# Kernel tuning notes

Measured on AMD Instinct MI355X. Metric: run time of the kernel, lower is better.

Reference implementation:

```python
import jax, jax.numpy as jnp
import numpy as np

DIM = 128
HEADS = 2
SR = 8
LN_EPS = 1e-5


def setup_inputs() -> dict:
    key = jax.random.key(0)
    ks = jax.random.split(key, 8)
    B, H, W, C = 8, 128, 128, DIM
    s = 0.02
    return {
        "x": jax.random.normal(ks[0], (B, H * W, C), jnp.float32),
        "h": H,
        "w": W,
        "Wq": jax.random.normal(ks[1], (C, C), jnp.float32) * s,
        "bq": jnp.zeros((C,), jnp.float32),
        "Wkv": jax.random.normal(ks[2], (2 * C, C), jnp.float32) * s,
        "bkv": jnp.zeros((2 * C,), jnp.float32),
        "Wp": jax.random.normal(ks[3], (C, C), jnp.float32) * s,
        "bp": jnp.zeros((C,), jnp.float32),
        "Wsr": jax.random.normal(ks[4], (C, C, SR, SR), jnp.float32) * s,  # OIHW
        "bsr": jnp.zeros((C,), jnp.float32),
        "gamma": jnp.ones((C,), jnp.float32),
        "beta": jnp.zeros((C,), jnp.float32),
    }


def reference(x, h, w, Wq, bq, Wkv, bkv, Wp, bp, Wsr, bsr, gamma, beta):
    b, n, c = x.shape
    hd = c // HEADS
    scale = hd ** -0.5
    # q: [b, heads, n, hd]
    q = (jnp.einsum('bnc,oc->bno', x, Wq) + bq).reshape(b, n, HEADS, hd).transpose(0, 2, 1, 3)
    # spatial reduction of k/v source: conv stride SR, then LayerNorm
    x_img = x.reshape(b, h, w, c).transpose(0, 3, 1, 2)  # NCHW
    xr = jax.lax.conv_general_dilated(
        x_img, Wsr, window_strides=(SR, SR), padding='VALID',
        dimension_numbers=('NCHW', 'OIHW', 'NCHW')) + bsr[None, :, None, None]
    xr = xr.reshape(b, c, -1).transpose(0, 2, 1)  # [b, m, c], m = (h/SR)*(w/SR)
    mu = jnp.mean(xr, axis=-1, keepdims=True)
    var = jnp.var(xr, axis=-1, keepdims=True)
    xr = (xr - mu) / jnp.sqrt(var + LN_EPS) * gamma + beta
    # k, v: [b, heads, m, hd]
    kv = jnp.einsum('bmc,oc->bmo', xr, Wkv) + bkv
    m = kv.shape[1]
    kv = kv.reshape(b, m, 2, HEADS, hd).transpose(2, 0, 3, 1, 4)
    k, v = kv[0], kv[1]
    attn = jax.nn.softmax(jnp.einsum('bhnd,bhmd->bhnm', q, k) * scale, axis=-1)
    out = jnp.einsum('bhnm,bhmd->bhnd', attn, v).transpose(0, 2, 1, 3).reshape(b, n, c)
    return jnp.einsum('bnc,oc->bno', out, Wp) + bp
```

## Files before the change

### kernel.cpp

```cpp
#include <hip/hip_runtime.h>
#include <stdint.h>

typedef __attribute__((ext_vector_type(8))) short bf16x8;
typedef __attribute__((ext_vector_type(4))) float f32x4;

#define MFMA16(A, B, C) __builtin_amdgcn_mfma_f32_16x16x32_bf16(A, B, C, 0, 0, 0)

static __device__ __forceinline__ unsigned short f2bf(float f) {
  uint32_t u = __float_as_uint(f);
  u = (u + 0x7fffu + ((u >> 16) & 1u)) >> 16;
  return (unsigned short)u;
}

static __device__ __forceinline__ bf16x8 pack8(float4 a, float4 b) {
  bf16x8 r;
  r[0] = (short)f2bf(a.x); r[1] = (short)f2bf(a.y);
  r[2] = (short)f2bf(a.z); r[3] = (short)f2bf(a.w);
  r[4] = (short)f2bf(b.x); r[5] = (short)f2bf(b.y);
  r[6] = (short)f2bf(b.z); r[7] = (short)f2bf(b.w);
  return r;
}

__global__ __launch_bounds__(256) void xcast_prep_kernel(
    const float* __restrict__ x, const float* __restrict__ Wq, const float* __restrict__ Wkv,
    const float* __restrict__ Wp, const float* __restrict__ Wsr,
    unsigned short* __restrict__ x2, unsigned short* __restrict__ x3,
    unsigned short* __restrict__ Wq2, unsigned short* __restrict__ Wkv2,
    unsigned short* __restrict__ Wp2, unsigned short* __restrict__ W2sr) {
  const int bid = blockIdx.x;
  const int tid = threadIdx.x;
  if (bid < 8192) {
    size_t t = (size_t)bid * 256 + tid;
    const float4* xp = (const float4*)(x + t * 8);
    bf16x8 v = pack8(xp[0], xp[1]);
    int n_all = (int)(t >> 4);
    int b = n_all >> 14, n = n_all & 16383;
    int c8 = (int)(t & 15);
    int c5 = c8 >> 2, c31 = (c8 & 3) * 8;
    size_t i2 = (size_t)b * 2097152 + ((size_t)((n >> 4) * 4 + c5)) * 512 + (n & 15) * 32 + c31;
    *(bf16x8*)(x2 + i2) = v;
    int y = n >> 7, xx = n & 127, jj = xx >> 3, kw = xx & 7;
    size_t i3 = (size_t)(b * 128 + y) * 16384 + ((size_t)(kw * 4 + c5)) * 512 + jj * 32 + c31;
    *(bf16x8*)(x3 + i3) = v;
    return;
  }
  if (bid < 8256) {
    int t = (bid - 8192) * 256 + tid;
    int o = t >> 7, c = t & 127;
    const float4* wp = (const float4*)(Wsr + (size_t)t * 64);
#pragma unroll
    for (int s4 = 0; s4 < 16; ++s4) {
      float4 v = wp[s4];
#pragma unroll
      for (int e = 0; e < 4; ++e) {
        int s = s4 * 4 + e;
        float f = (e == 0) ? v.x : (e == 1) ? v.y : (e == 2) ? v.z : v.w;
        W2sr[(size_t)((s * 4 + (c >> 5)) * 128 + o) * 32 + (c & 31)] = f2bf(f);
      }
    }
    return;
  }
  {
    int t = (bid - 8256) * 256 + tid;
    if (t < 16384) {
      int o = t >> 7, c = t & 127;
      Wq2[((c >> 5) * 128 + o) * 32 + (c & 31)] = f2bf(Wq[t]);
    } else if (t < 32768) {
      int u = t - 16384;
      int o = u >> 7, c = u & 127;
      Wp2[((c >> 5) * 128 + o) * 32 + (c & 31)] = f2bf(Wp[u]);
    } else {
      int u = t - 32768;
      int o = u >> 7, c = u & 127;
      Wkv2[((c >> 5) * 256 + o) * 32 + (c & 31)] = f2bf(Wkv[u]);
    }
  }
}

__global__ __launch_bounds__(256, 4) void conv_split_kernel(
    const unsigned short* __restrict__ x3, const unsigned short* __restrict__ W2sr,
    float* __restrict__ scratch) {
  const int tid = threadIdx.x;
  const int wave = tid >> 6, l = tid & 63, lg = l >> 4, lr = l & 15;
  const int pt = blockIdx.x;
  const int ks = blockIdx.y;

  __shared__ float red[4][16][128];

  const f32x4 zr = {0.f, 0.f, 0.f, 0.f};
  f32x4 acc[8];
#pragma unroll
  for (int ct = 0; ct < 8; ++ct) acc[ct] = zr;

  const int p = pt * 16;
  const int b = p >> 8, ii = (p >> 4) & 15;

  for (int kt = 0; kt < 16; ++kt) {
    const int k = ks * 2048 + wave * 512 + kt * 32;
    const int s = k >> 7, c0t = (k >> 5) & 3;
    const int kh = s >> 3, kw = s & 7, y = ii * 8 + kh;
    bf16x8 af = *(const bf16x8*)(x3 + (size_t)(b * 128 + y) * 16384 + (kw * 4 + c0t) * 512 + lr * 32 + lg * 8);
    const unsigned short* wb = W2sr + (size_t)(k >> 5) * 4096;
#pragma unroll
    for (int ct = 0; ct < 8; ++ct) {
      bf16x8 bfr = *(const bf16x8*)(wb + (ct * 16 + lr) * 32 + lg * 8);
      acc[ct] = MFMA16(af, bfr, acc[ct]);
    }
  }

#pragma unroll
  for (int ct = 0; ct < 8; ++ct)
#pragma unroll
    for (int r = 0; r < 4; ++r)
      red[wave][lg * 4 + r][ct * 16 + lr] = acc[ct][r];
  __syncthreads();

#pragma unroll
  for (int rr = 0; rr < 8; ++rr) {
    int idx = rr * 256 + tid;
    int row = idx >> 7, c = idx & 127;
    float v = red[0][row][c] + red[1][row][c] + red[2][row][c] + red[3][row][c];
    scratch[((size_t)(ks * 2048 + pt * 16 + row)) * 128 + c] = v;
  }
}

__global__ __launch_bounds__(256, 2) void ln_kv_kernel(
    const float* __restrict__ scratch, const float* __restrict__ bsr,
    const float* __restrict__ gamma, const float* __restrict__ beta,
    const unsigned short* __restrict__ Wkv2, const float* __restrict__ bkv,
    unsigned short* __restrict__ K2, unsigned short* __restrict__ V2) {
  const int tid = threadIdx.x;
  const int wave = tid >> 6, l = tid & 63, lg = l >> 4, lr = l & 15;
  const int blk = blockIdx.x;

  __shared__ unsigned short lns[16][136];

  {
    const int row = tid >> 4, c0 = (tid & 15) * 8;
    const int p = blk * 16 + row;
    float vals[8];
#pragma unroll
    for (int cc = 0; cc < 8; ++cc) vals[cc] = bsr[c0 + cc];
#pragma unroll
    for (int ksp = 0; ksp < 4; ++ksp) {
      const float4* sp = (const float4*)(scratch + ((size_t)(ksp * 2048 + p)) * 128 + c0);
      float4 a = sp[0], bb = sp[1];
      vals[0] += a.x; vals[1] += a.y; vals[2] += a.z; vals[3] += a.w;
      vals[4] += bb.x; vals[5] += bb.y; vals[6] += bb.z; vals[7] += bb.w;
    }
    float s1 = 0.f, s2 = 0.f;
#pragma unroll
    for (int cc = 0; cc < 8; ++cc) { s1 += vals[cc]; s2 += vals[cc] * vals[cc]; }
#pragma unroll
    for (int msk = 1; msk < 16; msk <<= 1) { s1 += __shfl_xor(s1, msk); s2 += __shfl_xor(s2, msk); }
    float mean = s1 * (1.f / 128.f);
    float var = s2 * (1.f / 128.f) - mean * mean;
    float rstd = rsqrtf(var + 1e-5f);
#pragma unroll
    for (int cc = 0; cc < 8; ++cc) {
      int c = c0 + cc;
      lns[row][c] = f2bf((vals[cc] - mean) * rstd * gamma[c] + beta[c]);
    }
  }
  __syncthreads();

  const f32x4 zr = {0.f, 0.f, 0.f, 0.f};
  f32x4 kv[4];
#pragma unroll
  for (int q = 0; q < 4; ++q) kv[q] = zr;
#pragma unroll
  for (int kt = 0; kt < 4; ++kt) {
    bf16x8 af = *(const bf16x8*)(&lns[lr][kt * 32 + lg * 8]);
#pragma unroll
    for (int q = 0; q < 4; ++q) {
      bf16x8 bfr = *(const bf16x8*)(Wkv2 + (kt * 256 + (wave * 4 + q) * 16 + lr) * 32 + lg * 8);
      kv[q] = MFMA16(af, bfr, kv[q]);
    }
  }
#pragma unroll
  for (int q = 0; q < 4; ++q)
#pragma unroll
    for (int r = 0; r < 4; ++r) {
      int o2 = (wave * 4 + q) * 16 + lr;
      int mrow = lg * 4 + r;
      int pp = blk * 16 + mrow;
      int bb = pp >> 8, mm = pp & 255;
      float val = kv[q][r] + bkv[o2];
      unsigned short hv = f2bf(val);
      if (o2 < 128) {
        int h = o2 >> 6, d = o2 & 63;
        K2[((size_t)((bb * 2 + h) * 2 + (d >> 5)) * 256 + mm) * 32 + (d & 31)] = hv;
      } else {
        int o3 = o2 - 128, h = o3 >> 6, d = o3 & 63;
        V2[((size_t)((bb * 2 + h) * 8 + (mm >> 5)) * 64 + d) * 32 + (mm & 31)] = hv;
      }
    }
}

__global__ __launch_bounds__(256, 3) void attn_kernel(
    const unsigned short* __restrict__ x2, const float* __restrict__ bq, const float* __restrict__ bp,
    const unsigned short* __restrict__ Wq2, const unsigned short* __restrict__ Wp2,
    const unsigned short* __restrict__ K2, const unsigned short* __restrict__ V2,
    float* __restrict__ out) {
  const int tid = threadIdx.x;
  const int wave = tid >> 6, l = tid & 63, lg = l >> 4, lr = l & 15;
  const int b = blockIdx.y;
  const int n0 = blockIdx.x * 64;

  __shared__ unsigned short Qs[64][136];
  __shared__ unsigned short Ps[4][16][272];

  const f32x4 zr = {0.f, 0.f, 0.f, 0.f};

  {
    const unsigned short* xbase = x2 + (size_t)b * 2097152 + (size_t)((n0 + wave * 16) >> 4) * 2048;
    bf16x8 af[4];
#pragma unroll
    for (int kt = 0; kt < 4; ++kt)
      af[kt] = *(const bf16x8*)(xbase + kt * 512 + lr * 32 + lg * 8);
    f32x4 qa[8];
#pragma unroll
    for (int ct = 0; ct < 8; ++ct) qa[ct] = zr;
#pragma unroll
    for (int kt = 0; kt < 4; ++kt) {
#pragma unroll
      for (int ct = 0; ct < 8; ++ct) {
        bf16x8 bfr = *(const bf16x8*)(Wq2 + (kt * 128 + ct * 16 + lr) * 32 + lg * 8);
        qa[ct] = MFMA16(af[kt], bfr, qa[ct]);
      }
    }
#pragma unroll
    for (int ct = 0; ct < 8; ++ct)
#pragma unroll
      for (int r = 0; r < 4; ++r) {
        int row = wave * 16 + lg * 4 + r;
        int col = ct * 16 + lr;
        Qs[row][col] = f2bf((qa[ct][r] + bq[col]) * 0.125f);
      }
  }
  __syncthreads();

  f32x4 oacc[2][4];
#pragma unroll
  for (int h2 = 0; h2 < 2; ++h2)
#pragma unroll
    for (int dt = 0; dt < 4; ++dt) oacc[h2][dt] = zr;

  for (int h = 0; h < 2; ++h) {
    f32x4 sacc[16];
#pragma unroll
    for (int mt = 0; mt < 16; ++mt) sacc[mt] = zr;
#pragma unroll
    for (int d0 = 0; d0 < 64; d0 += 32) {
      const unsigned short* kbase = K2 + (size_t)((b * 2 + h) * 2 + (d0 >> 5)) * 8192;
      bf16x8 qf = *(const bf16x8*)(&Qs[wave * 16 + lr][h * 64 + d0 + lg * 8]);
#pragma unroll
      for (int mt = 0; mt < 16; ++mt) {
        bf16x8 kf = *(const bf16x8*)(kbase + (mt * 16 + lr) * 32 + lg * 8);
        sacc[mt] = MFMA16(kf, qf, sacc[mt]);
      }
    }
    float mx = -1e30f;
#pragma unroll
    for (int mt = 0; mt < 16; ++mt)
#pragma unroll
      for (int r = 0; r < 4; ++r) mx = fmaxf(mx, sacc[mt][r]);
    mx = fmaxf(mx, __shfl_xor(mx, 16));
    mx = fmaxf(mx, __shfl_xor(mx, 32));
    float sum = 0.f;
#pragma unroll
    for (int mt = 0; mt < 16; ++mt)
#pragma unroll
      for (int r = 0; r < 4; ++r) {
        float pv = __expf(sacc[mt][r] - mx);
        sacc[mt][r] = pv; sum += pv;
      }
    sum += __shfl_xor(sum, 16);
    sum += __shfl_xor(sum, 32);
    float inv = 1.f / sum;
#pragma unroll
    for (int mt = 0; mt < 16; ++mt) {
      unsigned int w0 = (unsigned int)f2bf(sacc[mt][0] * inv) | ((unsigned int)f2bf(sacc[mt][1] * inv) << 16);
      unsigned int w1 = (unsigned int)f2bf(sacc[mt][2] * inv) | ((unsigned int)f2bf(sacc[mt][3] * inv) << 16);
      uint2 pw; pw.x = w0; pw.y = w1;
      *(uint2*)(&Ps[wave][lr][mt * 16 + lg * 4]) = pw;
    }

#pragma unroll
    for (int ki = 0; ki < 8; ++ki) {
      const unsigned short* vbase = V2 + (size_t)((b * 2 + h) * 8 + ki) * 2048;
      bf16x8 pf = *(const bf16x8*)(&Ps[wave][lr][ki * 32 + lg * 8]);
#pragma unroll
      for (int dt = 0; dt < 4; ++dt) {
        bf16x8 vf = *(const bf16x8*)(vbase + (dt * 16 + lr) * 32 + lg * 8);
        oacc[h][dt] = MFMA16(pf, vf, oacc[h][dt]);
      }
    }
  }

  __syncthreads();
  unsigned short* Op = &Ps[0][0][0];
#pragma unroll
  for (int h = 0; h < 2; ++h)
#pragma unroll
    for (int dt = 0; dt < 4; ++dt)
#pragma unroll
      for (int r = 0; r < 4; ++r) {
        int row = wave * 16 + lg * 4 + r;
        int col = h * 64 + dt * 16 + lr;
        Op[row * 136 + col] = f2bf(oacc[h][dt][r]);
      }

  f32x4 yacc[8];
#pragma unroll
  for (int ct = 0; ct < 8; ++ct) yacc[ct] = zr;
#pragma unroll
  for (int kt = 0; kt < 4; ++kt) {
    bf16x8 af = *(const bf16x8*)(&Op[(wave * 16 + lr) * 136 + kt * 32 + lg * 8]);
#pragma unroll
    for (int ct = 0; ct < 8; ++ct) {
      bf16x8 bfr = *(const bf16x8*)(Wp2 + (kt * 128 + ct * 16 + lr) * 32 + lg * 8);
      yacc[ct] = MFMA16(af, bfr, yacc[ct]);
    }
  }
#pragma unroll
  for (int ct = 0; ct < 8; ++ct)
#pragma unroll
    for (int r = 0; r < 4; ++r) {
      int n = n0 + wave * 16 + lg * 4 + r;
      int o = ct * 16 + lr;
      out[((size_t)(b * 16384 + n)) * 128 + o] = yacc[ct][r] + bp[o];
    }
}

extern "C" void kernel_launch(void* const* d_in, const int* in_sizes, int n_in,
                              void* d_out, int out_size, void* d_ws, size_t ws_size,
                              hipStream_t stream) {
  const float* x = (const float*)d_in[0];
  const float* Wq = (const float*)d_in[3];
  const float* bq = (const float*)d_in[4];
  const float* Wkv = (const float*)d_in[5];
  const float* bkv = (const float*)d_in[6];
  const float* Wp = (const float*)d_in[7];
  const float* bp = (const float*)d_in[8];
  const float* Wsr = (const float*)d_in[9];
  const float* bsr = (const float*)d_in[10];
  const float* gamma = (const float*)d_in[11];
  const float* beta = (const float*)d_in[12];
  float* out = (float*)d_out;

  unsigned short* ws = (unsigned short*)d_ws;
  unsigned short* Wq2 = ws;
  unsigned short* Wp2 = ws + 16384;
  unsigned short* Wkv2 = ws + 32768;
  unsigned short* W2sr = ws + 65536;
  unsigned short* K2 = ws + 1114112;
  unsigned short* V2 = ws + 1376256;
  unsigned short* x2 = ws + 1638400;
  unsigned short* x3 = ws + 18415616;
  float* scratch = (float*)(ws + 35192832);

  xcast_prep_kernel<<<8512, 256, 0, stream>>>(x, Wq, Wkv, Wp, Wsr, x2, x3, Wq2, Wkv2, Wp2, W2sr);
  conv_split_kernel<<<dim3(128, 4), 256, 0, stream>>>(x3, W2sr, scratch);
  ln_kv_kernel<<<128, 256, 0, stream>>>(scratch, bsr, gamma, beta, Wkv2, bkv, K2, V2);
  attn_kernel<<<dim3(256, 8), 256, 0, stream>>>(x2, bq, bp, Wq2, Wp2, K2, V2, out);
}
```

Measured before the change: 286.4 us.

## Drop bf16 x staging buffers; cast x in-kernel in conv and attention

Removes the prep pass that converted x into two bf16 layouts (x2, x3) in global memory. The conv and attention kernels now read fp32 x directly, convert it to bf16 in shared memory (with an XOR swizzle in conv), and the conv writes per-wave partial sums that ln_kv reduces over 16 splits. The attention kernel switches to per-wave shared buffers with lgkmcnt waits instead of block barriers, and stages the output through LDS for coalesced float4 stores. This saves about 64MB of intermediate writes and reads, at the cost of more scratch traffic and more LDS per conv block.

```diff
diff --git a/kernel.cpp b/kernel.cpp
--- a/kernel.cpp
+++ b/kernel.cpp
@@ -5,6 +5,9 @@
 typedef __attribute__((ext_vector_type(4))) float f32x4;
 
 #define MFMA16(A, B, C) __builtin_amdgcn_mfma_f32_16x16x32_bf16(A, B, C, 0, 0, 0)
+
+#define LGKM_GUARD() do { asm volatile("s_waitcnt lgkmcnt(0)" ::: "memory"); \
+                          __builtin_amdgcn_sched_barrier(0); } while (0)
 
 static __device__ __forceinline__ unsigned short f2bf(float f) {
   uint32_t u = __float_as_uint(f);
@@ -21,31 +24,15 @@
   return r;
 }
 
-__global__ __launch_bounds__(256) void xcast_prep_kernel(
-    const float* __restrict__ x, const float* __restrict__ Wq, const float* __restrict__ Wkv,
+__global__ __launch_bounds__(256) void prep_kernel(
+    const float* __restrict__ Wq, const float* __restrict__ Wkv,
     const float* __restrict__ Wp, const float* __restrict__ Wsr,
-    unsigned short* __restrict__ x2, unsigned short* __restrict__ x3,
     unsigned short* __restrict__ Wq2, unsigned short* __restrict__ Wkv2,
     unsigned short* __restrict__ Wp2, unsigned short* __restrict__ W2sr) {
   const int bid = blockIdx.x;
   const int tid = threadIdx.x;
-  if (bid < 8192) {
-    size_t t = (size_t)bid * 256 + tid;
-    const float4* xp = (const float4*)(x + t * 8);
-    bf16x8 v = pack8(xp[0], xp[1]);
-    int n_all = (int)(t >> 4);
-    int b = n_all >> 14, n = n_all & 16383;
-    int c8 = (int)(t & 15);
-    int c5 = c8 >> 2, c31 = (c8 & 3) * 8;
-    size_t i2 = (size_t)b * 2097152 + ((size_t)((n >> 4) * 4 + c5)) * 512 + (n & 15) * 32 + c31;
-    *(bf16x8*)(x2 + i2) = v;
-    int y = n >> 7, xx = n & 127, jj = xx >> 3, kw = xx & 7;
-    size_t i3 = (size_t)(b * 128 + y) * 16384 + ((size_t)(kw * 4 + c5)) * 512 + jj * 32 + c31;
-    *(bf16x8*)(x3 + i3) = v;
-    return;
-  }
-  if (bid < 8256) {
-    int t = (bid - 8192) * 256 + tid;
+  if (bid < 64) {
+    int t = bid * 256 + tid;
     int o = t >> 7, c = t & 127;
     const float4* wp = (const float4*)(Wsr + (size_t)t * 64);
 #pragma unroll
@@ -60,46 +47,57 @@
     }
     return;
   }
-  {
-    int t = (bid - 8256) * 256 + tid;
-    if (t < 16384) {
-      int o = t >> 7, c = t & 127;
-      Wq2[((c >> 5) * 128 + o) * 32 + (c & 31)] = f2bf(Wq[t]);
-    } else if (t < 32768) {
-      int u = t - 16384;
-      int o = u >> 7, c = u & 127;
-      Wp2[((c >> 5) * 128 + o) * 32 + (c & 31)] = f2bf(Wp[u]);
-    } else {
-      int u = t - 32768;
-      int o = u >> 7, c = u & 127;
-      Wkv2[((c >> 5) * 256 + o) * 32 + (c & 31)] = f2bf(Wkv[u]);
-    }
-  }
-}
-
-__global__ __launch_bounds__(256, 4) void conv_split_kernel(
-    const unsigned short* __restrict__ x3, const unsigned short* __restrict__ W2sr,
+  int t = (bid - 64) * 256 + tid;
+  if (t < 16384) {
+    int o = t >> 7, c = t & 127;
+    Wq2[((c >> 5) * 128 + o) * 32 + (c & 31)] = f2bf(Wq[t]);
+  } else if (t < 32768) {
+    int u = t - 16384;
+    int o = u >> 7, c = u & 127;
+    Wp2[((c >> 5) * 128 + o) * 32 + (c & 31)] = f2bf(Wp[u]);
+  } else {
+    int u = t - 32768;
+    int o = u >> 7, c = u & 127;
+    Wkv2[((c >> 5) * 256 + o) * 32 + (c & 31)] = f2bf(Wkv[u]);
+  }
+}
+
+__global__ __launch_bounds__(256, 2) void conv_split_kernel(
+    const float* __restrict__ x, const unsigned short* __restrict__ W2sr,
     float* __restrict__ scratch) {
   const int tid = threadIdx.x;
   const int wave = tid >> 6, l = tid & 63, lg = l >> 4, lr = l & 15;
   const int pt = blockIdx.x;
   const int ks = blockIdx.y;
-
-  __shared__ float red[4][16][128];
+  const int b = pt >> 4, ii = pt & 15;
+
+  __shared__ __align__(16) unsigned short Xc[2][16384];
+
+  const float* src = x + (size_t)b * 2097152 + (size_t)(ii * 8 + ks * 2) * 16384;
+#pragma unroll
+  for (int it = 0; it < 32; ++it) {
+    int f = it * 1024 + tid * 4;
+    float4 v = *(const float4*)(src + f);
+    int row = f >> 14, o = f & 16383;
+    int byteoff = (o * 2) ^ (((o >> 10) & 7) << 4);
+    ushort4 h;
+    h.x = f2bf(v.x); h.y = f2bf(v.y); h.z = f2bf(v.z); h.w = f2bf(v.w);
+    *(ushort4*)((char*)&Xc[row][0] + byteoff) = h;
+  }
+  __syncthreads();
 
   const f32x4 zr = {0.f, 0.f, 0.f, 0.f};
   f32x4 acc[8];
 #pragma unroll
   for (int ct = 0; ct < 8; ++ct) acc[ct] = zr;
-
-  const int p = pt * 16;
-  const int b = p >> 8, ii = (p >> 4) & 15;
 
   for (int kt = 0; kt < 16; ++kt) {
     const int k = ks * 2048 + wave * 512 + kt * 32;
     const int s = k >> 7, c0t = (k >> 5) & 3;
-    const int kh = s >> 3, kw = s & 7, y = ii * 8 + kh;
-    bf16x8 af = *(const bf16x8*)(x3 + (size_t)(b * 128 + y) * 16384 + (kw * 4 + c0t) * 512 + lr * 32 + lg * 8);
+    const int kw = s & 7, yl = (s >> 3) & 1;
+    int o_r = (lr * 8 + kw) * 128 + c0t * 32 + lg * 8;
+    int byteoff = (o_r * 2) ^ ((lr & 7) << 4);
+    bf16x8 af = *(const bf16x8*)((const char*)&Xc[yl][0] + byteoff);
     const unsigned short* wb = W2sr + (size_t)(k >> 5) * 4096;
 #pragma unroll
     for (int ct = 0; ct < 8; ++ct) {
@@ -112,16 +110,7 @@
   for (int ct = 0; ct < 8; ++ct)
 #pragma unroll
     for (int r = 0; r < 4; ++r)
-      red[wave][lg * 4 + r][ct * 16 + lr] = acc[ct][r];
-  __syncthreads();
-
-#pragma unroll
-  for (int rr = 0; rr < 8; ++rr) {
-    int idx = rr * 256 + tid;
-    int row = idx >> 7, c = idx & 127;
-    float v = red[0][row][c] + red[1][row][c] + red[2][row][c] + red[3][row][c];
-    scratch[((size_t)(ks * 2048 + pt * 16 + row)) * 128 + c] = v;
-  }
+      scratch[((size_t)((ks * 4 + wave) * 2048 + pt * 16 + lg * 4 + r)) * 128 + ct * 16 + lr] = acc[ct][r];
 }
 
 __global__ __launch_bounds__(256, 2) void ln_kv_kernel(
@@ -142,7 +131,7 @@
 #pragma unroll
     for (int cc = 0; cc < 8; ++cc) vals[cc] = bsr[c0 + cc];
 #pragma unroll
-    for (int ksp = 0; ksp < 4; ++ksp) {
+    for (int ksp = 0; ksp < 16; ++ksp) {
       const float4* sp = (const float4*)(scratch + ((size_t)(ksp * 2048 + p)) * 128 + c0);
       float4 a = sp[0], bb = sp[1];
       vals[0] += a.x; vals[1] += a.y; vals[2] += a.z; vals[3] += a.w;
@@ -198,47 +187,59 @@
 }
 
 __global__ __launch_bounds__(256, 3) void attn_kernel(
-    const unsigned short* __restrict__ x2, const float* __restrict__ bq, const float* __restrict__ bp,
+    const float* __restrict__ x, const float* __restrict__ bq, const float* __restrict__ bp,
     const unsigned short* __restrict__ Wq2, const unsigned short* __restrict__ Wp2,
     const unsigned short* __restrict__ K2, const unsigned short* __restrict__ V2,
     float* __restrict__ out) {
   const int tid = threadIdx.x;
   const int wave = tid >> 6, l = tid & 63, lg = l >> 4, lr = l & 15;
   const int b = blockIdx.y;
-  const int n0 = blockIdx.x * 64;
-
-  __shared__ unsigned short Qs[64][136];
-  __shared__ unsigned short Ps[4][16][272];
+  const int n0 = blockIdx.x * 64 + wave * 16;
+
+  __shared__ __align__(16) unsigned short XQ[4][16 * 136];
+  __shared__ __align__(16) unsigned short PS[4][16 * 264];
+
+  unsigned short* Xs = &XQ[wave][0];
+  unsigned short* Ps = &PS[wave][0];
 
   const f32x4 zr = {0.f, 0.f, 0.f, 0.f};
 
   {
-    const unsigned short* xbase = x2 + (size_t)b * 2097152 + (size_t)((n0 + wave * 16) >> 4) * 2048;
+    const float* src = x + ((size_t)b * 16384 + n0) * 128;
+#pragma unroll
+    for (int q = 0; q < 8; ++q) {
+      int f = q * 256 + l * 4;
+      float4 v = *(const float4*)(src + f);
+      int row = f >> 7, col = f & 127;
+      ushort4 h;
+      h.x = f2bf(v.x); h.y = f2bf(v.y); h.z = f2bf(v.z); h.w = f2bf(v.w);
+      *(ushort4*)(Xs + row * 136 + col) = h;
+    }
+  }
+  LGKM_GUARD();
+
+  {
     bf16x8 af[4];
 #pragma unroll
     for (int kt = 0; kt < 4; ++kt)
-      af[kt] = *(const bf16x8*)(xbase + kt * 512 + lr * 32 + lg * 8);
+      af[kt] = *(const bf16x8*)(Xs + lr * 136 + kt * 32 + lg * 8);
+    LGKM_GUARD();
     f32x4 qa[8];
 #pragma unroll
     for (int ct = 0; ct < 8; ++ct) qa[ct] = zr;
 #pragma unroll
-    for (int kt = 0; kt < 4; ++kt) {
+    for (int kt = 0; kt < 4; ++kt)
 #pragma unroll
       for (int ct = 0; ct < 8; ++ct) {
         bf16x8 bfr = *(const bf16x8*)(Wq2 + (kt * 128 + ct * 16 + lr) * 32 + lg * 8);
         qa[ct] = MFMA16(af[kt], bfr, qa[ct]);
       }
-    }
 #pragma unroll
     for (int ct = 0; ct < 8; ++ct)
 #pragma unroll
-      for (int r = 0; r < 4; ++r) {
-        int row = wave * 16 + lg * 4 + r;
-        int col = ct * 16 + lr;
-        Qs[row][col] = f2bf((qa[ct][r] + bq[col]) * 0.125f);
-      }
-  }
-  __syncthreads();
+      for (int r = 0; r < 4; ++r)
+        Xs[(lg * 4 + r) * 136 + ct * 16 + lr] = f2bf((qa[ct][r] + bq[ct * 16 + lr]) * 0.125f);
+  }
 
   f32x4 oacc[2][4];
 #pragma unroll
@@ -253,7 +254,7 @@
 #pragma unroll
     for (int d0 = 0; d0 < 64; d0 += 32) {
       const unsigned short* kbase = K2 + (size_t)((b * 2 + h) * 2 + (d0 >> 5)) * 8192;
-      bf16x8 qf = *(const bf16x8*)(&Qs[wave * 16 + lr][h * 64 + d0 + lg * 8]);
+      bf16x8 qf = *(const bf16x8*)(Xs + lr * 136 + h * 64 + d0 + lg * 8);
 #pragma unroll
       for (int mt = 0; mt < 16; ++mt) {
         bf16x8 kf = *(const bf16x8*)(kbase + (mt * 16 + lr) * 32 + lg * 8);
@@ -278,18 +279,19 @@
     sum += __shfl_xor(sum, 16);
     sum += __shfl_xor(sum, 32);
     float inv = 1.f / sum;
+    if (h == 1) LGKM_GUARD();
 #pragma unroll
     for (int mt = 0; mt < 16; ++mt) {
       unsigned int w0 = (unsigned int)f2bf(sacc[mt][0] * inv) | ((unsigned int)f2bf(sacc[mt][1] * inv) << 16);
       unsigned int w1 = (unsigned int)f2bf(sacc[mt][2] * inv) | ((unsigned int)f2bf(sacc[mt][3] * inv) << 16);
       uint2 pw; pw.x = w0; pw.y = w1;
-      *(uint2*)(&Ps[wave][lr][mt * 16 + lg * 4]) = pw;
+      *(uint2*)(Ps + lr * 264 + mt * 16 + lg * 4) = pw;
     }
 
 #pragma unroll
     for (int ki = 0; ki < 8; ++ki) {
       const unsigned short* vbase = V2 + (size_t)((b * 2 + h) * 8 + ki) * 2048;
-      bf16x8 pf = *(const bf16x8*)(&Ps[wave][lr][ki * 32 + lg * 8]);
+      bf16x8 pf = *(const bf16x8*)(Ps + lr * 264 + ki * 32 + lg * 8);
 #pragma unroll
       for (int dt = 0; dt < 4; ++dt) {
         bf16x8 vf = *(const bf16x8*)(vbase + (dt * 16 + lr) * 32 + lg * 8);
@@ -298,39 +300,48 @@
     }
   }
 
-  __syncthreads();
-  unsigned short* Op = &Ps[0][0][0];
+  LGKM_GUARD();
 #pragma unroll
   for (int h = 0; h < 2; ++h)
 #pragma unroll
     for (int dt = 0; dt < 4; ++dt)
 #pragma unroll
-      for (int r = 0; r < 4; ++r) {
-        int row = wave * 16 + lg * 4 + r;
-        int col = h * 64 + dt * 16 + lr;
-        Op[row * 136 + col] = f2bf(oacc[h][dt][r]);
-      }
-
+      for (int r = 0; r < 4; ++r)
+        Ps[(lg * 4 + r) * 136 + h * 64 + dt * 16 + lr] = f2bf(oacc[h][dt][r]);
+
+  bf16x8 af2[4];
+#pragma unroll
+  for (int kt = 0; kt < 4; ++kt)
+    af2[kt] = *(const bf16x8*)(Ps + lr * 136 + kt * 32 + lg * 8);
+  LGKM_GUARD();
   f32x4 yacc[8];
 #pragma unroll
   for (int ct = 0; ct < 8; ++ct) yacc[ct] = zr;
 #pragma unroll
-  for (int kt = 0; kt < 4; ++kt) {
-    bf16x8 af = *(const bf16x8*)(&Op[(wave * 16 + lr) * 136 + kt * 32 + lg * 8]);
+  for (int kt = 0; kt < 4; ++kt)
 #pragma unroll
     for (int ct = 0; ct < 8; ++ct) {
       bf16x8 bfr = *(const bf16x8*)(Wp2 + (kt * 128 + ct * 16 + lr) * 32 + lg * 8);
-      yacc[ct] = MFMA16(af, bfr, yacc[ct]);
-    }
-  }
+      yacc[ct] = MFMA16(af2[kt], bfr, yacc[ct]);
+    }
+
+  float* Osf = (float*)Ps;
 #pragma unroll
   for (int ct = 0; ct < 8; ++ct)
 #pragma unroll
-    for (int r = 0; r < 4; ++r) {
-      int n = n0 + wave * 16 + lg * 4 + r;
-      int o = ct * 16 + lr;
-      out[((size_t)(b * 16384 + n)) * 128 + o] = yacc[ct][r] + bp[o];
-    }
+    for (int r = 0; r < 4; ++r)
+      Osf[(lg * 4 + r) * 132 + ct * 16 + lr] = yacc[ct][r] + bp[ct * 16 + lr];
+
+  {
+    float* dst = out + ((size_t)b * 16384 + n0) * 128;
+#pragma unroll
+    for (int q = 0; q < 8; ++q) {
+      int f = q * 256 + l * 4;
+      int row = f >> 7, col = f & 127;
+      float4 v = *(const float4*)(Osf + row * 132 + col);
+      *(float4*)(dst + f) = v;
+    }
+  }
 }
 
 extern "C" void kernel_launch(void* const* d_in, const int* in_sizes, int n_in,
@@ -356,12 +367,10 @@
   unsigned short* W2sr = ws + 65536;
   unsigned short* K2 = ws + 1114112;
   unsigned short* V2 = ws + 1376256;
-  unsigned short* x2 = ws + 1638400;
-  unsigned short* x3 = ws + 18415616;
-  float* scratch = (float*)(ws + 35192832);
-
-  xcast_prep_kernel<<<8512, 256, 0, stream>>>(x, Wq, Wkv, Wp, Wsr, x2, x3, Wq2, Wkv2, Wp2, W2sr);
-  conv_split_kernel<<<dim3(128, 4), 256, 0, stream>>>(x3, W2sr, scratch);
+  float* scratch = (float*)(ws + 1638400);
+
+  prep_kernel<<<320, 256, 0, stream>>>(Wq, Wkv, Wp, Wsr, Wq2, Wkv2, Wp2, W2sr);
+  conv_split_kernel<<<dim3(128, 4), 256, 0, stream>>>(x, W2sr, scratch);
   ln_kv_kernel<<<128, 256, 0, stream>>>(scratch, bsr, gamma, beta, Wkv2, bkv, K2, V2);
-  attn_kernel<<<dim3(256, 8), 256, 0, stream>>>(x2, bq, bp, Wq2, Wp2, K2, V2, out);
-}
+  attn_kernel<<<dim3(256, 8), 256, 0, stream>>>(x, bq, bp, Wq2, Wp2, K2, V2, out);
+}
```

Result: slower. 321.7 us (+12.3%).
